# Performance work log

Hardware: AMD Instinct MI355X
Metric: run time of the kernel (lower is better)

The kernel has to match this reference:

```python
import jax, jax.numpy as jnp
import numpy as np

EPS = 1e-5
GROUPS = 16
OUT_CH = 128
GC = OUT_CH // GROUPS  # group_channels = 8
SPAN = 128


def _bn(x, gamma, beta, axes):
    # BatchNorm in training mode: biased batch statistics over `axes`.
    m = jnp.mean(x, axis=axes, keepdims=True)
    v = jnp.var(x, axis=axes, keepdims=True)
    shape = [1] * x.ndim
    shape[1] = x.shape[1]
    g = gamma.reshape(shape)
    b = beta.reshape(shape)
    return (x - m) * jax.lax.rsqrt(v + EPS) * g + b


def setup_inputs() -> dict:
    key = jax.random.key(0)
    ks = jax.random.split(key, 3)
    x = jax.random.normal(ks[0], (2, 128, 64, 128), dtype=jnp.float32)
    W_qkv = jax.random.normal(ks[1], (2 * OUT_CH, 128), dtype=jnp.float32) * (1.0 / np.sqrt(128))
    rel_emb = jax.random.normal(ks[2], (2 * GC, 2 * SPAN - 1), dtype=jnp.float32)
    return {
        "x": x,
        "W_qkv": W_qkv,
        "gamma_qkv": jnp.ones((2 * OUT_CH,), jnp.float32),
        "beta_qkv": jnp.zeros((2 * OUT_CH,), jnp.float32),
        "rel_emb": rel_emb,
        "gamma_sim": jnp.ones((3 * GROUPS,), jnp.float32),
        "beta_sim": jnp.zeros((3 * GROUPS,), jnp.float32),
        "gamma_out": jnp.ones((2 * OUT_CH,), jnp.float32),
        "beta_out": jnp.zeros((2 * OUT_CH,), jnp.float32),
    }


def reference(x, W_qkv, gamma_qkv, beta_qkv, rel_emb, gamma_sim, beta_sim, gamma_out, beta_out):
    # dim == 1: attend over the width axis. x: [B, C, H, W], W == SPAN.
    B, C, H, W = x.shape
    xr = jnp.transpose(x, (0, 2, 1, 3)).reshape(B * H, C, W)  # [BH, C, W]

    # 1x1 Conv1d + BN1d -> query/key/value
    qkv = jnp.einsum('oc,bcl->bol', W_qkv, xr)  # [BH, 2*OUT, W]
    qkv = _bn(qkv, gamma_qkv, beta_qkv, axes=(0, 2))
    qkv = qkv.reshape(B * H, GROUPS, 2 * GC, W)
    q = qkv[:, :, : GC // 2]            # [BH, g, gc/2, W]
    k = qkv[:, :, GC // 2: GC]          # [BH, g, gc/2, W]
    v = qkv[:, :, GC:]                  # [BH, g, gc,   W]

    # relative position embeddings gathered into [2*gc, span, span]
    idx = jnp.arange(SPAN)[:, None] - jnp.arange(SPAN)[None, :] + SPAN - 1
    emb = rel_emb[:, idx]               # [2*gc, span, span]
    q_emb = emb[: GC // 2]
    k_emb = emb[GC // 2: GC]
    v_emb = emb[GC:]

    qe = jnp.einsum('bgci,cij->bgij', q, q_emb)   # [BH, g, W, W]
    ke = jnp.einsum('bgci,cij->bgij', k, k_emb)   # [BH, g, W, W]
    # faithful to original: contracts the first spatial axis of qe/ke
    qk = jnp.einsum('bgci,bgcj->bgij', qe, ke)    # [BH, g, W, W]

    sim = jnp.concatenate([qk, qe, ke], axis=1)   # [BH, 3g, W, W]
    sim = _bn(sim, gamma_sim, beta_sim, axes=(0, 2, 3))
    sim = sim.reshape(B * H, 3, GROUPS, W, W).sum(axis=1)  # [BH, g, W, W]
    sim = jax.nn.softmax(sim, axis=3)

    am = jnp.einsum('bgij,bgcj->bgci', sim, v)      # [BH, g, gc, W]
    ame = jnp.einsum('bgij,cij->bgci', sim, v_emb)  # [BH, g, gc, W]

    out = jnp.concatenate([am, ame], axis=-1).reshape(B * H, 2 * OUT_CH, W)
    out = _bn(out, gamma_out, beta_out, axes=(0, 2))
    out = out.reshape(B, H, OUT_CH, 2, W).sum(axis=-2)  # [B, H, OUT, W]
    return jnp.transpose(out, (0, 2, 1, 3))             # [B, OUT, H, W]
```

## Files before the change

kernel.cpp:

```cpp
#include <hip/hip_runtime.h>

#define EPS 1e-5f
typedef unsigned short u16;
typedef unsigned int u32;

typedef __attribute__((ext_vector_type(8))) short bf16x8;
typedef __attribute__((ext_vector_type(4))) float f32x4;

__device__ __forceinline__ float bf2f(u16 h) {
    u32 u = ((u32)h) << 16;
    return __builtin_bit_cast(float, u);
}
__device__ __forceinline__ u16 f2bf(float f) {
    u32 u = __builtin_bit_cast(u32, f);
    u32 r = (u + 0x7fffu + ((u >> 16) & 1u)) >> 16;
    return (u16)r;
}
__device__ __forceinline__ u32 pack2(float a, float b) {
    return (u32)f2bf(a) | ((u32)f2bf(b) << 16);
}

__global__ __launch_bounds__(256) void k1_gemm_qkv(
    const float* __restrict__ x, const float* __restrict__ Wq,
    float* __restrict__ qkv, float* __restrict__ stats)
{
    __shared__ float Wt[64 * 68];
    __shared__ float xt[64 * 128];
    const int tid = threadIdx.x;
    const int ot = blockIdx.x;
    const int n  = blockIdx.y;
    const int b = n >> 6, h = n & 63;
    const int to = tid >> 5, tl = tid & 31;
    const int o0 = to * 8, l0 = tl * 4;

    float acc[8][4];
#pragma unroll
    for (int r = 0; r < 8; ++r) { acc[r][0]=0.f; acc[r][1]=0.f; acc[r][2]=0.f; acc[r][3]=0.f; }

    for (int cb = 0; cb < 128; cb += 64) {
        __syncthreads();
#pragma unroll
        for (int k = 0; k < 4; ++k) {
            int f = tid + k * 256;
            int oo = f >> 4, c4 = f & 15;
            float4 v = *(const float4*)(Wq + (ot * 64 + oo) * 128 + cb + c4 * 4);
            *(float4*)(Wt + oo * 68 + c4 * 4) = v;
        }
#pragma unroll
        for (int k = 0; k < 8; ++k) {
            int f = tid + k * 256;
            int c = f >> 5, l4 = f & 31;
            float4 v = *(const float4*)(x + ((size_t)((b * 128 + cb + c) * 64 + h)) * 128 + l4 * 4);
            *(float4*)(xt + c * 128 + l4 * 4) = v;
        }
        __syncthreads();
#pragma unroll 4
        for (int c = 0; c < 64; ++c) {
            float4 xv = *(const float4*)(xt + c * 128 + l0);
#pragma unroll
            for (int r = 0; r < 8; ++r) {
                float w = Wt[(o0 + r) * 68 + c];
                acc[r][0] += w * xv.x; acc[r][1] += w * xv.y;
                acc[r][2] += w * xv.z; acc[r][3] += w * xv.w;
            }
        }
    }

#pragma unroll
    for (int r = 0; r < 8; ++r) {
        int o = ot * 64 + o0 + r;
        *(float4*)(qkv + ((size_t)n * 256 + o) * 128 + l0) =
            make_float4(acc[r][0], acc[r][1], acc[r][2], acc[r][3]);
        float s  = acc[r][0] + acc[r][1] + acc[r][2] + acc[r][3];
        float sq = acc[r][0]*acc[r][0] + acc[r][1]*acc[r][1] + acc[r][2]*acc[r][2] + acc[r][3]*acc[r][3];
#pragma unroll
        for (int m = 1; m < 32; m <<= 1) {
            s  += __shfl_xor(s, m);
            sq += __shfl_xor(sq, m);
        }
        if (tl == 0) {
            atomicAdd(&stats[o], s);
            atomicAdd(&stats[256 + o], sq);
        }
    }
}

__global__ void k3_coef_qkv(const float* __restrict__ stats,
                            const float* __restrict__ gamma, const float* __restrict__ beta,
                            float* __restrict__ coef)
{
    int o = threadIdx.x;
    const float cnt = 16384.f;
    float mean = stats[o] / cnt;
    float var  = stats[256 + o] / cnt - mean * mean;
    float a = gamma[o] * rsqrtf(var + EPS);
    coef[o] = a;
    coef[256 + o] = beta[o] - a * mean;
}

__global__ __launch_bounds__(512, 4) void k4_pass1(
    const float* __restrict__ qkv, const float* __restrict__ rel,
    const float* __restrict__ cq, u16* __restrict__ qk,
    float* __restrict__ stats)
{
    __shared__ u16 QEb[128 * 136];
    __shared__ u16 KEb[128 * 136];
    __shared__ float red[8 * 6];
    const int tid = threadIdx.x;
    const int n = blockIdx.x >> 4, g = blockIdx.x & 15;

    const int pt = tid & 31, pi = tid >> 5;
    const int t0 = pt * 4, i0 = pi * 8;
    const int d0 = t0 - i0 + 120;

    float qes = 0.f, qesq = 0.f, kes = 0.f, kesq = 0.f;

#pragma unroll
    for (int mat = 0; mat < 2; ++mat) {
        float qv[4][4];
#pragma unroll
        for (int c = 0; c < 4; ++c) {
            int o = g * 16 + mat * 4 + c;
            float a = cq[o], bb = cq[256 + o];
            float4 x0 = *(const float4*)(qkv + ((size_t)n * 256 + o) * 128 + t0);
            qv[c][0] = fmaf(a, x0.x, bb); qv[c][1] = fmaf(a, x0.y, bb);
            qv[c][2] = fmaf(a, x0.z, bb); qv[c][3] = fmaf(a, x0.w, bb);
        }
        float rr[4][12];
#pragma unroll
        for (int c = 0; c < 4; ++c) {
            const float* p = rel + (mat * 4 + c) * 255 + d0;
#pragma unroll
            for (int j = 0; j < 3; ++j) {
                float4 v = *(const float4*)(p + j * 4);
                rr[c][j*4+0] = v.x; rr[c][j*4+1] = v.y;
                rr[c][j*4+2] = v.z; rr[c][j*4+3] = v.w;
            }
        }
        u16* MB = mat ? KEb : QEb;
        float s = 0.f, sq = 0.f;
#pragma unroll
        for (int ii = 0; ii < 8; ++ii) {
            float vv[4];
#pragma unroll
            for (int tt = 0; tt < 4; ++tt) {
                int dl = tt - ii + 7;
                float v = qv[0][tt] * rr[0][dl] + qv[1][tt] * rr[1][dl]
                        + qv[2][tt] * rr[2][dl] + qv[3][tt] * rr[3][dl];
                vv[tt] = v;
                s += v; sq = fmaf(v, v, sq);
            }
            *(uint2*)(MB + (i0 + ii) * 136 + t0) =
                make_uint2(pack2(vv[0], vv[1]), pack2(vv[2], vv[3]));
        }
        if (mat == 0) { qes = s; qesq = sq; } else { kes = s; kesq = sq; }
    }
    __syncthreads();

    const int lane = tid & 63, wv = tid >> 6;
    const int fm = lane & 15, fq = lane >> 4;

    f32x4 acc[8];
#pragma unroll
    for (int tj = 0; tj < 8; ++tj) acc[tj] = (f32x4){0.f, 0.f, 0.f, 0.f};

#pragma unroll
    for (int kb = 0; kb < 4; ++kb) {
        const int ko = kb * 32 + fq * 8;
        bf16x8 a0 = *(const bf16x8*)(QEb + (wv * 16 + fm) * 136 + ko);
#pragma unroll
        for (int tj = 0; tj < 8; ++tj) {
            bf16x8 bfr = *(const bf16x8*)(KEb + (tj * 16 + fm) * 136 + ko);
            acc[tj] = __builtin_amdgcn_mfma_f32_16x16x32_bf16(a0, bfr, acc[tj], 0, 0, 0);
        }
    }

    float qks = 0.f, qksq = 0.f;
#pragma unroll
    for (int tj = 0; tj < 8; ++tj) {
#pragma unroll
        for (int r = 0; r < 4; ++r) {
            float v = acc[tj][r];
            qks += v; qksq = fmaf(v, v, qksq);
            QEb[(wv * 16 + fq * 4 + r) * 136 + tj * 16 + fm] = f2bf(v);
        }
    }

#pragma unroll
    for (int m = 1; m < 64; m <<= 1) {
        qes += __shfl_xor(qes, m);  qesq += __shfl_xor(qesq, m);
        kes += __shfl_xor(kes, m);  kesq += __shfl_xor(kesq, m);
        qks += __shfl_xor(qks, m);  qksq += __shfl_xor(qksq, m);
    }
    if (lane == 0) {
        red[wv * 6 + 0] = qes; red[wv * 6 + 1] = qesq;
        red[wv * 6 + 2] = kes; red[wv * 6 + 3] = kesq;
        red[wv * 6 + 4] = qks; red[wv * 6 + 5] = qksq;
    }
    __syncthreads();

    u16* qkg = qk + (size_t)(n * 16 + g) * 16384;
#pragma unroll
    for (int k = 0; k < 4; ++k) {
        int f = tid + k * 512;
        int row = f >> 4, c8 = f & 15;
        uint4 v = *(const uint4*)(QEb + row * 136 + c8 * 8);
        *(uint4*)(qkg + row * 128 + c8 * 8) = v;
    }

    if (tid < 6) {
        float tot = 0.f;
#pragma unroll
        for (int w = 0; w < 8; ++w) tot += red[w * 6 + tid];
        int off = (tid & 1) ? 560 : 512;
        int ch = (tid < 2) ? (16 + g) : (tid < 4) ? (32 + g) : g;
        atomicAdd(&stats[off + ch], tot);
    }
}

__global__ void k5_coef_sim(const float* __restrict__ stats,
                            const float* __restrict__ gamma, const float* __restrict__ beta,
                            float* __restrict__ coef)
{
    int ch = threadIdx.x;
    if (ch < 48) {
        const float cnt = 2097152.f;
        float mean = stats[512 + ch] / cnt;
        float var  = stats[560 + ch] / cnt - mean * mean;
        float a = gamma[ch] * rsqrtf(var + EPS);
        coef[ch] = a;
        coef[48 + ch] = beta[ch] - a * mean;
    }
}

#define K6_STEP(rb, rv, vv, jl)                                              \
    {                                                                        \
        float qe = q0 * bf2f((u16)rb[0]) + q1 * bf2f((u16)rb[1])             \
                 + q2 * bf2f((u16)rb[2]) + q3 * bf2f((u16)rb[3]);            \
        float ke = k0 * bf2f((u16)rb[4]) + k1 * bf2f((u16)rb[5])             \
                 + k2 * bf2f((u16)rb[6]) + k3 * bf2f((u16)rb[7]);            \
        float s = fmaf(aqk, bf2f(qh.hh[jl]), qe + ke + bsum);                \
        float e = __expf(s);                                                 \
        l += e;                                                              \
        _Pragma("unroll")                                                    \
        for (int c = 0; c < 8; ++c) {                                        \
            am[c]  = fmaf(e, bf2f((u16)vv[c]), am[c]);                       \
            ame[c] = fmaf(e, bf2f((u16)rv[c]), ame[c]);                      \
        }                                                                    \
    }

__global__ __launch_bounds__(128, 4) void k6_pass2(
    const float* __restrict__ qkv, const float* __restrict__ rel,
    const float* __restrict__ cq, const float* __restrict__ cs,
    const u16* __restrict__ qk,
    float* __restrict__ outraw, float* __restrict__ ostats)
{
    __shared__ u16 relb[256 * 24];
    __shared__ u16 vb[128 * 8];
    __shared__ float qn_s[8 * 128];
    const int tid = threadIdx.x;
    const int n = blockIdx.x >> 4, g = blockIdx.x & 15;

#pragma unroll
    for (int k = 0; k < 32; ++k) {
        int f = tid + k * 128;
        int c = f >> 8, d = f & 255;
        if (d < 255) relb[d * 24 + c] = f2bf(rel[c * 255 + d]);
    }
#pragma unroll
    for (int k = 0; k < 8; ++k) {
        int f = tid + k * 128;
        int c = f >> 7, t = f & 127;
        int o = g * 16 + c;
        qn_s[f] = fmaf(cq[o], qkv[((size_t)n * 256 + o) * 128 + t], cq[256 + o]);
    }
#pragma unroll
    for (int k = 0; k < 8; ++k) {
        int f = tid + k * 128;
        int c = f >> 7, j = f & 127;
        int o = g * 16 + 8 + c;
        float v = fmaf(cq[o], qkv[((size_t)n * 256 + o) * 128 + j], cq[256 + o]);
        vb[j * 8 + c] = f2bf(v);
    }
    __syncthreads();

    const float aqk = cs[g], aqe = cs[16 + g], ake = cs[32 + g];
    const float bsum = cs[48 + g] + cs[64 + g] + cs[80 + g];
    const int i = tid;

    float q0 = aqe * qn_s[i],       q1 = aqe * qn_s[128 + i];
    float q2 = aqe * qn_s[256 + i], q3 = aqe * qn_s[384 + i];
    float k0 = ake * qn_s[512 + i], k1 = ake * qn_s[640 + i];
    float k2 = ake * qn_s[768 + i], k3 = ake * qn_s[896 + i];

    const u16* qkrow = qk + (size_t)(n * 16 + g) * 16384 + i * 128;

    float l = 0.f;
    float am[8], ame[8];
#pragma unroll
    for (int c = 0; c < 8; ++c) { am[c] = 0.f; ame[c] = 0.f; }

#pragma unroll
    for (int jc = 0; jc < 8; ++jc) {
        union { uint4 v[2]; u16 hh[16]; } qh;
        qh.v[0] = *(const uint4*)(qkrow + jc * 16);
        qh.v[1] = *(const uint4*)(qkrow + jc * 16 + 8);

        const int dbase = i + 127 - jc * 16;
#pragma unroll
        for (int js = 0; js < 4; ++js) {
            const int dd = dbase - js * 4;
            const int jj = jc * 16 + js * 4;
            bf16x8 rb0 = *(const bf16x8*)(relb + (dd    ) * 24);
            bf16x8 rb1 = *(const bf16x8*)(relb + (dd - 1) * 24);
            bf16x8 rb2 = *(const bf16x8*)(relb + (dd - 2) * 24);
            bf16x8 rb3 = *(const bf16x8*)(relb + (dd - 3) * 24);
            bf16x8 rv0 = *(const bf16x8*)(relb + (dd    ) * 24 + 8);
            bf16x8 rv1 = *(const bf16x8*)(relb + (dd - 1) * 24 + 8);
            bf16x8 rv2 = *(const bf16x8*)(relb + (dd - 2) * 24 + 8);
            bf16x8 rv3 = *(const bf16x8*)(relb + (dd - 3) * 24 + 8);
            bf16x8 vv0 = *(const bf16x8*)(vb + (jj + 0) * 8);
            bf16x8 vv1 = *(const bf16x8*)(vb + (jj + 1) * 8);
            bf16x8 vv2 = *(const bf16x8*)(vb + (jj + 2) * 8);
            bf16x8 vv3 = *(const bf16x8*)(vb + (jj + 3) * 8);

            K6_STEP(rb0, rv0, vv0, js * 4 + 0);
            K6_STEP(rb1, rv1, vv1, js * 4 + 1);
            K6_STEP(rb2, rv2, vv2, js * 4 + 2);
            K6_STEP(rb3, rv3, vv3, js * 4 + 3);
        }
    }

    float inv = 1.f / l;
    float o16[16];
#pragma unroll
    for (int c = 0; c < 8; ++c) { o16[2 * c] = am[c] * inv; o16[2 * c + 1] = ame[c] * inv; }

    float* orow = outraw + ((size_t)n * 256 + g * 16) * 128 + i;
#pragma unroll
    for (int c16 = 0; c16 < 16; ++c16) orow[c16 * 128] = o16[c16];

    const int lane = tid & 63;
#pragma unroll
    for (int c16 = 0; c16 < 16; ++c16) {
        float sv = o16[c16], sq = o16[c16] * o16[c16];
#pragma unroll
        for (int mm = 1; mm < 64; mm <<= 1) { sv += __shfl_xor(sv, mm); sq += __shfl_xor(sq, mm); }
        if (lane == 0) {
            atomicAdd(&ostats[g * 16 + c16], sv);
            atomicAdd(&ostats[256 + g * 16 + c16], sq);
        }
    }
}

__global__ void k7_coef_out(const float* __restrict__ stats,
                            const float* __restrict__ gamma, const float* __restrict__ beta,
                            float* __restrict__ coef)
{
    int o = threadIdx.x;
    const float cnt = 16384.f;
    float mean = stats[608 + o] / cnt;
    float var  = stats[864 + o] / cnt - mean * mean;
    float a = gamma[o] * rsqrtf(var + EPS);
    coef[o] = a;
    coef[256 + o] = beta[o] - a * mean;
}

__global__ __launch_bounds__(256) void k8_final(
    const float* __restrict__ outraw, const float* __restrict__ co,
    float* __restrict__ out)
{
    int idx = blockIdx.x * 256 + threadIdx.x;
    int w  = idx & 127;
    int h  = (idx >> 7) & 63;
    int oc = (idx >> 13) & 127;
    int b  = idx >> 20;
    int n  = b * 64 + h;
    int o0 = oc * 2;
    float x0 = outraw[((size_t)n * 256 + o0) * 128 + w];
    float x1 = outraw[((size_t)n * 256 + o0 + 1) * 128 + w];
    out[idx] = (co[o0] * x0 + co[256 + o0]) + (co[o0 + 1] * x1 + co[256 + o0 + 1]);
}

extern "C" void kernel_launch(void* const* d_in, const int* in_sizes, int n_in,
                              void* d_out, int out_size, void* d_ws, size_t ws_size,
                              hipStream_t stream)
{
    const float* x   = (const float*)d_in[0];
    const float* Wq  = (const float*)d_in[1];
    const float* gq  = (const float*)d_in[2];
    const float* bq  = (const float*)d_in[3];
    const float* rel = (const float*)d_in[4];
    const float* gs  = (const float*)d_in[5];
    const float* bs  = (const float*)d_in[6];
    const float* go  = (const float*)d_in[7];
    const float* bo  = (const float*)d_in[8];

    float* ws     = (float*)d_ws;
    float* qkv    = ws;
    float* outraw = ws + 4194304;
    u16*   qk     = (u16*)(ws + 8388608);
    float* stats  = ws + 25165824;
    float* cq     = stats + 1120;
    float* cs     = stats + 1632;
    float* co     = stats + 1728;

    (void)hipMemsetAsync(stats, 0, 1120 * sizeof(float), stream);

    k1_gemm_qkv<<<dim3(4, 128), 256, 0, stream>>>(x, Wq, qkv, stats);
    k3_coef_qkv<<<1, 256, 0, stream>>>(stats, gq, bq, cq);
    k4_pass1<<<2048, 512, 0, stream>>>(qkv, rel, cq, qk, stats);
    k5_coef_sim<<<1, 64, 0, stream>>>(stats, gs, bs, cs);
    k6_pass2<<<2048, 128, 0, stream>>>(qkv, rel, cq, cs, qk, outraw, stats + 608);
    k7_coef_out<<<1, 256, 0, stream>>>(stats, go, bo, co);
    k8_final<<<8192, 256, 0, stream>>>(outraw, co, (float*)d_out);
}
```

Before: 333.5 us.

## Split pass2 rows across two blocks and key range across thread pairs

The attention-apply kernel now launches two blocks per (batch-row, group), each covering half of the query rows. Within a block, two adjacent threads split the 128 keys of one query row. The partial softmax sums and accumulators are combined with a lane-xor shuffle, and the relative-embedding shared buffer shrinks to the 192 diagonals each block needs. This halves the serial per-thread loop and doubles the number of waves, so there is more parallelism for latency hiding. In exchange, the v tile is loaded redundantly per block and the stats atomics double.

```diff
diff --git a/kernel.cpp b/kernel.cpp
--- a/kernel.cpp
+++ b/kernel.cpp
@@ -255,24 +255,28 @@
     const u16* __restrict__ qk,
     float* __restrict__ outraw, float* __restrict__ ostats)
 {
-    __shared__ u16 relb[256 * 24];
+    __shared__ u16 relb[192 * 24];
     __shared__ u16 vb[128 * 8];
-    __shared__ float qn_s[8 * 128];
+    __shared__ float qn_s[512];
     const int tid = threadIdx.x;
-    const int n = blockIdx.x >> 4, g = blockIdx.x & 15;
-
-#pragma unroll
-    for (int k = 0; k < 32; ++k) {
+    const int bx = blockIdx.x;
+    const int n = bx >> 5, g = (bx >> 1) & 15, rh = bx & 1;
+    const int il = tid >> 1, h = tid & 1;
+    const int i = rh * 64 + il;
+
+#pragma unroll
+    for (int k = 0; k < 24; ++k) {
         int f = tid + k * 128;
-        int c = f >> 8, d = f & 255;
-        if (d < 255) relb[d * 24 + c] = f2bf(rel[c * 255 + d]);
-    }
-#pragma unroll
-    for (int k = 0; k < 8; ++k) {
+        int dloc = f >> 4, c = f & 15;
+        int d = rh * 64 + dloc;
+        if (d < 255) relb[dloc * 24 + c] = f2bf(rel[c * 255 + d]);
+    }
+#pragma unroll
+    for (int k = 0; k < 4; ++k) {
         int f = tid + k * 128;
-        int c = f >> 7, t = f & 127;
+        int c = f >> 6, r2 = f & 63;
         int o = g * 16 + c;
-        qn_s[f] = fmaf(cq[o], qkv[((size_t)n * 256 + o) * 128 + t], cq[256 + o]);
+        qn_s[f] = fmaf(cq[o], qkv[((size_t)n * 256 + o) * 128 + rh * 64 + r2], cq[256 + o]);
     }
 #pragma unroll
     for (int k = 0; k < 8; ++k) {
@@ -286,14 +290,13 @@
 
     const float aqk = cs[g], aqe = cs[16 + g], ake = cs[32 + g];
     const float bsum = cs[48 + g] + cs[64 + g] + cs[80 + g];
-    const int i = tid;
-
-    float q0 = aqe * qn_s[i],       q1 = aqe * qn_s[128 + i];
-    float q2 = aqe * qn_s[256 + i], q3 = aqe * qn_s[384 + i];
-    float k0 = ake * qn_s[512 + i], k1 = ake * qn_s[640 + i];
-    float k2 = ake * qn_s[768 + i], k3 = ake * qn_s[896 + i];
-
-    const u16* qkrow = qk + (size_t)(n * 16 + g) * 16384 + i * 128;
+
+    float q0 = aqe * qn_s[il],       q1 = aqe * qn_s[64 + il];
+    float q2 = aqe * qn_s[128 + il], q3 = aqe * qn_s[192 + il];
+    float k0 = ake * qn_s[256 + il], k1 = ake * qn_s[320 + il];
+    float k2 = ake * qn_s[384 + il], k3 = ake * qn_s[448 + il];
+
+    const u16* qkrow = qk + (size_t)(n * 16 + g) * 16384 + i * 128 + h * 64;
 
     float l = 0.f;
     float am[8], ame[8];
@@ -301,16 +304,17 @@
     for (int c = 0; c < 8; ++c) { am[c] = 0.f; ame[c] = 0.f; }
 
 #pragma unroll
-    for (int jc = 0; jc < 8; ++jc) {
+    for (int jc = 0; jc < 4; ++jc) {
         union { uint4 v[2]; u16 hh[16]; } qh;
         qh.v[0] = *(const uint4*)(qkrow + jc * 16);
         qh.v[1] = *(const uint4*)(qkrow + jc * 16 + 8);
 
-        const int dbase = i + 127 - jc * 16;
+        const int dbase = il + 127 - h * 64 - jc * 16;
+        const int jb = h * 64 + jc * 16;
 #pragma unroll
         for (int js = 0; js < 4; ++js) {
             const int dd = dbase - js * 4;
-            const int jj = jc * 16 + js * 4;
+            const int jj = jb + js * 4;
             bf16x8 rb0 = *(const bf16x8*)(relb + (dd    ) * 24);
             bf16x8 rb1 = *(const bf16x8*)(relb + (dd - 1) * 24);
             bf16x8 rb2 = *(const bf16x8*)(relb + (dd - 2) * 24);
@@ -331,24 +335,32 @@
         }
     }
 
-    float inv = 1.f / l;
-    float o16[16];
-#pragma unroll
-    for (int c = 0; c < 8; ++c) { o16[2 * c] = am[c] * inv; o16[2 * c + 1] = ame[c] * inv; }
-
-    float* orow = outraw + ((size_t)n * 256 + g * 16) * 128 + i;
-#pragma unroll
-    for (int c16 = 0; c16 < 16; ++c16) orow[c16 * 128] = o16[c16];
-
-    const int lane = tid & 63;
-#pragma unroll
-    for (int c16 = 0; c16 < 16; ++c16) {
-        float sv = o16[c16], sq = o16[c16] * o16[c16];
-#pragma unroll
-        for (int mm = 1; mm < 64; mm <<= 1) { sv += __shfl_xor(sv, mm); sq += __shfl_xor(sq, mm); }
-        if (lane == 0) {
-            atomicAdd(&ostats[g * 16 + c16], sv);
-            atomicAdd(&ostats[256 + g * 16 + c16], sq);
+    l += __shfl_xor(l, 1);
+#pragma unroll
+    for (int c = 0; c < 8; ++c) {
+        am[c]  += __shfl_xor(am[c], 1);
+        ame[c] += __shfl_xor(ame[c], 1);
+    }
+
+    if (h == 0) {
+        float inv = 1.f / l;
+        float o16[16];
+#pragma unroll
+        for (int c = 0; c < 8; ++c) { o16[2 * c] = am[c] * inv; o16[2 * c + 1] = ame[c] * inv; }
+
+        float* orow = outraw + ((size_t)n * 256 + g * 16) * 128 + i;
+#pragma unroll
+        for (int c16 = 0; c16 < 16; ++c16) orow[c16 * 128] = o16[c16];
+
+#pragma unroll
+        for (int c16 = 0; c16 < 16; ++c16) {
+            float sv = o16[c16], sq = o16[c16] * o16[c16];
+#pragma unroll
+            for (int mm = 2; mm < 64; mm <<= 1) { sv += __shfl_xor(sv, mm); sq += __shfl_xor(sq, mm); }
+            if ((tid & 63) == 0) {
+                atomicAdd(&ostats[g * 16 + c16], sv);
+                atomicAdd(&ostats[256 + g * 16 + c16], sq);
+            }
         }
     }
 }
@@ -411,7 +423,7 @@
     k3_coef_qkv<<<1, 256, 0, stream>>>(stats, gq, bq, cq);
     k4_pass1<<<2048, 512, 0, stream>>>(qkv, rel, cq, qk, stats);
     k5_coef_sim<<<1, 64, 0, stream>>>(stats, gs, bs, cs);
-    k6_pass2<<<2048, 128, 0, stream>>>(qkv, rel, cq, cs, qk, outraw, stats + 608);
+    k6_pass2<<<4096, 128, 0, stream>>>(qkv, rel, cq, cs, qk, outraw, stats + 608);
     k7_coef_out<<<1, 256, 0, stream>>>(stats, go, bo, co);
     k8_final<<<8192, 256, 0, stream>>>(outraw, co, (float*)d_out);
 }
```

New measurement: 439.1 us. +31.7%, slower.
